# Optimization experiments

Hardware: AMD Instinct MI355X
Metric: run time of the kernel (lower is better)

## Reference

```python
import jax, jax.numpy as jnp
import numpy as np

B, S, H = 1, 2048, 1024
NH, NKV, D = 8, 2, 128           # query heads, kv heads, head_dim
E, TOPK = 64, 6                   # experts per modality, top-k
IT, IV, IS = 512, 256, 1024       # text / vision expert inter, shared inter (=512*2)
THETA = 500000.0
SECTIONS = (22, 22, 20)           # h, w, t rotary freq split; sum = D//2
EPS = 1e-5


def rmsnorm(x, w):
    return x * w * jax.lax.rsqrt(jnp.mean(x * x, axis=-1, keepdims=True) + EPS)


def apply_mrope(x, positions):
    # x: [B,S,h,D]; positions: [3,B,S] (h, w, t position streams)
    inv_freq = 1.0 / (THETA ** (jnp.arange(0, D, 2, dtype=jnp.float32) / D))  # [D//2]
    axis_idx = np.repeat(np.arange(3), SECTIONS)              # which pos stream per freq band
    pos = jnp.transpose(positions[axis_idx], (1, 2, 0)).astype(jnp.float32)  # [B,S,D//2]
    freqs = pos * inv_freq
    cos = jnp.cos(freqs)[:, :, None, :]
    sin = jnp.sin(freqs)[:, :, None, :]
    x1, x2 = x[..., 0::2], x[..., 1::2]                       # interleaved (non-neox)
    o1 = x1 * cos - x2 * sin
    o2 = x1 * sin + x2 * cos
    return jnp.stack([o1, o2], axis=-1).reshape(x.shape)


def attention(x, positions, w_qkv, w_o):
    b, s, _ = x.shape
    qkv = x @ w_qkv
    q, k, v = jnp.split(qkv, [NH * D, NH * D + NKV * D], axis=-1)
    q = q.reshape(b, s, NH, D)
    k = k.reshape(b, s, NKV, D)
    v = v.reshape(b, s, NKV, D)
    q = apply_mrope(q, positions)
    k = apply_mrope(k, positions)
    rep = NH // NKV
    k = jnp.repeat(k, rep, axis=2)
    v = jnp.repeat(v, rep, axis=2)
    scores = jnp.einsum('bqhd,bkhd->bhqk', q, k) * (D ** -0.5)
    causal = jnp.tril(jnp.ones((s, s), bool))
    scores = jnp.where(causal, scores, -jnp.inf)
    attn = jax.nn.softmax(scores, axis=-1)
    out = jnp.einsum('bhqk,bkhd->bqhd', attn, v).reshape(b, s, NH * D)
    return out @ w_o


def mlp(x, wg, wu, wd):
    return (jax.nn.silu(x @ wg) * (x @ wu)) @ wd


def moe_branch(x, gate_w, bias, wg, wu, wd):
    # x: [T,H]; gate_w: [H,E] fp32; bias: [E] fp32 correction bias
    logits = x.astype(jnp.float32) @ gate_w                   # [T,E]
    scores = jax.nn.sigmoid(logits)
    _, topi = jax.lax.top_k(scores + bias[None, :], TOPK)     # bias only picks experts
    w = jnp.take_along_axis(scores, topi, axis=-1)            # weights from raw scores
    w = w / jnp.sum(w, axis=-1, keepdims=True)                # renormalize
    T = x.shape[0]
    gates = jnp.zeros((T, E), jnp.float32).at[jnp.arange(T)[:, None], topi].set(w)
    g = jax.nn.silu(jnp.einsum('th,ehi->eti', x, wg)) * jnp.einsum('th,ehi->eti', x, wu)
    g = g * gates.T[:, :, None].astype(x.dtype)               # fold routing weights pre-down-proj
    return jnp.einsum('eti,eih->th', g, wd)


def _forward(hidden_states, positions, visual_token_mask, w_qkv, w_o, ln1_w, ln2_w,
             text_gate_w, vision_gate_w, corr_bias, tw_gate, tw_up, tw_down,
             vw_gate, vw_up, vw_down, sw_gate, sw_up, sw_down):
    h = hidden_states + attention(rmsnorm(hidden_states, ln1_w), positions, w_qkv, w_o)
    x = rmsnorm(h, ln2_w).reshape(-1, H)                      # [T,H]
    shared = mlp(x, sw_gate, sw_up, sw_down)
    text_out = moe_branch(x, text_gate_w, corr_bias[0], tw_gate, tw_up, tw_down)
    vision_out = moe_branch(x, vision_gate_w, corr_bias[1], vw_gate, vw_up, vw_down)
    mask = visual_token_mask.reshape(-1, 1)
    moe_out = jnp.where(mask, vision_out, text_out) + shared
    return h + moe_out.reshape(h.shape)


def setup_inputs() -> dict:
    key = jax.random.key(0)
    ks = jax.random.split(key, 16)
    rn = lambda i, shape, s: jax.random.normal(ks[i], shape, jnp.float32) * s
    return dict(
        hidden_states=rn(0, (B, S, H), 1.0),
        positions=jnp.broadcast_to(jnp.arange(S, dtype=jnp.int32)[None, None, :], (3, B, S)),
        visual_token_mask=jax.random.bernoulli(ks[1], 0.3, (B, S)),
        w_qkv=rn(2, (H, (NH + 2 * NKV) * D), H ** -0.5),
        w_o=rn(3, (NH * D, H), (NH * D) ** -0.5),
        ln1_w=jnp.ones((H,), jnp.float32),
        ln2_w=jnp.ones((H,), jnp.float32),
        text_gate_w=rn(4, (H, E), H ** -0.5),
        vision_gate_w=rn(5, (H, E), H ** -0.5),
        corr_bias=rn(6, (2, E), 0.02),
        tw_gate=rn(7, (E, H, IT), H ** -0.5),
        tw_up=rn(8, (E, H, IT), H ** -0.5),
        tw_down=rn(9, (E, IT, H), IT ** -0.5),
        vw_gate=rn(10, (E, H, IV), H ** -0.5),
        vw_up=rn(11, (E, H, IV), H ** -0.5),
        vw_down=rn(12, (E, IV, H), IV ** -0.5),
        sw_gate=rn(13, (H, IS), H ** -0.5),
        sw_up=rn(14, (H, IS), H ** -0.5),
        sw_down=rn(15, (IS, H), IS ** -0.5),
    )


def reference(hidden_states, positions, visual_token_mask, w_qkv, w_o, ln1_w, ln2_w,
              text_gate_w, vision_gate_w, corr_bias, tw_gate, tw_up, tw_down,
              vw_gate, vw_up, vw_down, sw_gate, sw_up, sw_down):
    return _forward(hidden_states, positions, visual_token_mask, w_qkv, w_o, ln1_w, ln2_w,
                    text_gate_w, vision_gate_w, corr_bias, tw_gate, tw_up, tw_down,
                    vw_gate, vw_up, vw_down, sw_gate, sw_up, sw_down)
```

## Files before the change

### kernel.cpp

```cpp
#include <hip/hip_runtime.h>
#include <hip/hip_bf16.h>
#include <math.h>

#define TT   2048
#define HID  1024
#define NHEAD 8
#define NKVH  2
#define HD   128
#define QKVN 1536
#define NEXP 64
#define NTOP 6
#define I_T  512
#define I_V  256
#define I_S  1024
#define SBASE ((size_t)12288 * 512)
#define NCHUNK 576

typedef unsigned short u16;
typedef __attribute__((ext_vector_type(8))) short short8v;
typedef __attribute__((ext_vector_type(4))) float f32x4;

__device__ inline u16 f2bf(float f) {
  __hip_bfloat16 h = __float2bfloat16(f);
  return *reinterpret_cast<u16*>(&h);
}
__device__ inline float bfu2f(u16 u) {
  unsigned x = ((unsigned)u) << 16;
  return __uint_as_float(x);
}
__device__ inline void split2(float f, u16& h, u16& l) {
  h = f2bf(f);
  l = f2bf(f - bfu2f(h));
}
__device__ inline void split8(const float* f, u16* h, u16* l) {
#pragma unroll
  for (int i = 0; i < 8; ++i) split2(f[i], h[i], l[i]);
}

__device__ inline f32x4 mfma16(short8v a, short8v b, f32x4 c) {
  return __builtin_amdgcn_mfma_f32_16x16x32_bf16(a, b, c, 0, 0, 0);
}

__device__ inline void wload64(const float* __restrict__ W, int ldw, int c0, int kc,
                               float4* r) {
  const int t = threadIdx.x;
  const int c4 = (t & 15) << 2;
  const int r0 = t >> 4;
#pragma unroll
  for (int j = 0; j < 8; ++j)
    r[j] = *(const float4*)&W[(size_t)(kc + r0 + j * 16) * ldw + c0 + c4];
}
__device__ inline void wwrite64(const float4* r, u16* lds) {
  const int t = threadIdx.x;
  const int c4 = (t & 15) << 2;
  const int r0 = t >> 4;
#pragma unroll
  for (int j = 0; j < 8; ++j) {
    int k = r0 + j * 16;
    u16* dst = lds + ((size_t)(k >> 3) * 64 + c4) * 8 + (k & 7);
    float4 v = r[j];
    dst[0]  = f2bf(v.x);
    dst[8]  = f2bf(v.y);
    dst[16] = f2bf(v.z);
    dst[24] = f2bf(v.w);
  }
}

template<bool F32, bool BF, bool LO>
__global__ __launch_bounds__(256) void rmsnorm_kernel(const float* __restrict__ x,
                                                      const float* __restrict__ w,
                                                      float* __restrict__ o32,
                                                      u16* __restrict__ obfH,
                                                      u16* __restrict__ obfL) {
  const int row = blockIdx.x;
  const int t = threadIdx.x;
  const float4 v = *(const float4*)(x + (size_t)row * HID + t * 4);
  float ss = v.x*v.x + v.y*v.y + v.z*v.z + v.w*v.w;
#pragma unroll
  for (int m = 32; m >= 1; m >>= 1) ss += __shfl_xor(ss, m);
  __shared__ float red[4];
  __shared__ float rrs;
  if ((t & 63) == 0) red[t >> 6] = ss;
  __syncthreads();
  if (t == 0) rrs = rsqrtf((red[0] + red[1] + red[2] + red[3]) * (1.0f / HID) + 1e-5f);
  __syncthreads();
  const float rr = rrs;
  const float4 wv = *(const float4*)(w + t * 4);
  float o[4];
  o[0] = v.x * wv.x * rr; o[1] = v.y * wv.y * rr;
  o[2] = v.z * wv.z * rr; o[3] = v.w * wv.w * rr;
  if (F32) *(float4*)(o32 + (size_t)row * HID + t * 4) = *(float4*)o;
  if (BF) {
    u16 h[4], l[4];
#pragma unroll
    for (int i = 0; i < 4; ++i) split2(o[i], h[i], l[i]);
    *(uint2*)(obfH + (size_t)row * HID + t * 4) = *(uint2*)h;
    if (LO) *(uint2*)(obfL + (size_t)row * HID + t * 4) = *(uint2*)l;
  }
}

__global__ __launch_bounds__(256) void convert_w(const float* __restrict__ W, int N,
                                                 u16* __restrict__ PH,
                                                 u16* __restrict__ PL) {
  const int c = blockIdx.x * 256 + threadIdx.x;
  const int k8 = blockIdx.y;
  float f[8];
#pragma unroll
  for (int e = 0; e < 8; ++e) f[e] = W[(size_t)(k8 * 8 + e) * N + c];
  u16 h8[8], l8[8];
  split8(f, h8, l8);
  size_t gi = ((size_t)(c >> 5) * 128 + k8) * 256 + (size_t)(c & 31) * 8;
  *(uint4*)&PH[gi] = *(uint4*)h8;
  *(uint4*)&PL[gi] = *(uint4*)l8;
}

template<bool RES>
__global__ __launch_bounds__(256) void dense_split(const u16* __restrict__ AH,
                                                   const u16* __restrict__ AL,
                                                   const u16* __restrict__ WPH,
                                                   const u16* __restrict__ WPL,
                                                   const float* __restrict__ resid,
                                                   float* __restrict__ C, int N) {
  __shared__ u16 sWH[32768], sWL[32768];
  __shared__ u16 sAH[4096],  sAL[4096];
  const int t = threadIdx.x;
  const int cs = blockIdx.x;
  const int c0 = cs * 32;
  const int rows = TT / gridDim.y;
  const int mstart = blockIdx.y * rows, mend = mstart + rows;
  {
    const u16* gh = WPH + (size_t)cs * 32768;
    const u16* gl = WPL + (size_t)cs * 32768;
#pragma unroll
    for (int r = 0; r < 16; ++r) {
      int i8 = (t + 256 * r) * 8;
      *(uint4*)&sWH[i8] = *(const uint4*)&gh[i8];
      *(uint4*)&sWL[i8] = *(const uint4*)&gl[i8];
    }
  }
  const int w = t >> 6, lane = t & 63;
  const int rowHalf = (w & 1) << 4, colHalf = (w >> 1) << 4;
  for (int m0 = mstart; m0 < mend; m0 += 32) {
    f32x4 hh = {0.f,0.f,0.f,0.f}, hl = {0.f,0.f,0.f,0.f};
    f32x4 lh = {0.f,0.f,0.f,0.f}, ll = {0.f,0.f,0.f,0.f};
    for (int kc = 0; kc < HID; kc += 128) {
      __syncthreads();
#pragma unroll
      for (int r = 0; r < 2; ++r) {
        int task = t + 256 * r;
        int row = task >> 4, kg = task & 15;
        size_t g = (size_t)(m0 + row) * HID + kc + kg * 8;
        *(uint4*)&sAH[(kg * 32 + row) * 8] = *(const uint4*)&AH[g];
        *(uint4*)&sAL[(kg * 32 + row) * 8] = *(const uint4*)&AL[g];
      }
      __syncthreads();
#pragma unroll
      for (int ks = 0; ks < 4; ++ks) {
        int arow = rowHalf + (lane & 15);
        int akg = ks * 4 + (lane >> 4);
        short8v ah = *(const short8v*)&sAH[(akg * 32 + arow) * 8];
        short8v al = *(const short8v*)&sAL[(akg * 32 + arow) * 8];
        int wcol = colHalf + (lane & 15);
        int wkg = (kc >> 3) + ks * 4 + (lane >> 4);
        short8v bh = *(const short8v*)&sWH[(wkg * 32 + wcol) * 8];
        short8v bl = *(const short8v*)&sWL[(wkg * 32 + wcol) * 8];
        hh = mfma16(ah, bh, hh);
        hl = mfma16(ah, bl, hl);
        lh = mfma16(al, bh, lh);
        ll = mfma16(al, bl, ll);
      }
    }
    f32x4 acc = (hh + hl) + (lh + ll);
#pragma unroll
    for (int i = 0; i < 4; ++i) {
      int r = m0 + rowHalf + ((lane >> 4) << 2) + i;
      int c = c0 + colHalf + (lane & 15);
      float v = acc[i];
      if (RES) v += resid[(size_t)r * N + c];
      C[(size_t)r * N + c] = v;
    }
  }
}

__global__ __launch_bounds__(256) void pack_qkv(const float* __restrict__ qkv,
                                                const int* __restrict__ pos,
                                                u16* __restrict__ Qh, u16* __restrict__ Ql,
                                                u16* __restrict__ Kph, u16* __restrict__ Kpl,
                                                u16* __restrict__ Vph, u16* __restrict__ Vpl) {
  const int tile = blockIdx.x;
  const int t = threadIdx.x;
  __shared__ float cs[2048], sn[2048];
  for (int i = t; i < 2048; i += 256) {
    int tok32 = i >> 6, fi = i & 63;
    int tok = tile * 32 + tok32;
    int axis = (fi < 22) ? 0 : (fi < 44 ? 1 : 2);
    float posv = (float)pos[axis * TT + tok];
    float invf = powf(500000.0f, -((float)(2 * fi)) / 128.0f);
    float ang = posv * invf;
    sincosf(ang, &sn[i], &cs[i]);
  }
  __syncthreads();
  for (int task = t; task < 4096; task += 256) {
    int h = task >> 9;
    int rem = task & 511;
    int tok32 = rem >> 4, fi4 = rem & 15;
    int tok = tile * 32 + tok32;
    const float* src = qkv + (size_t)tok * QKVN + h * HD + fi4 * 8;
    float4 v0 = *(const float4*)src, v1 = *(const float4*)(src + 4);
    float f[8] = {v0.x, v0.y, v0.z, v0.w, v1.x, v1.y, v1.z, v1.w};
    float o[8];
#pragma unroll
    for (int j = 0; j < 4; ++j) {
      int fi = fi4 * 4 + j;
      float c = cs[tok32 * 64 + fi], s = sn[tok32 * 64 + fi];
      o[2*j]   = f[2*j] * c - f[2*j+1] * s;
      o[2*j+1] = f[2*j] * s + f[2*j+1] * c;
    }
    u16 h8[8], l8[8];
    split8(o, h8, l8);
    size_t d = (size_t)tok * HID + h * HD + fi4 * 8;
    *(uint4*)&Qh[d] = *(uint4*)h8;
    *(uint4*)&Ql[d] = *(uint4*)l8;
  }
  for (int task = t; task < 1024; task += 256) {
    int kvh = task >> 9;
    int rem = task & 511;
    int kk = rem >> 4, fi4 = rem & 15;
    int tok = tile * 32 + kk;
    const float* src = qkv + (size_t)tok * QKVN + NHEAD * HD + kvh * HD + fi4 * 8;
    float4 v0 = *(const float4*)src, v1 = *(const float4*)(src + 4);
    float f[8] = {v0.x, v0.y, v0.z, v0.w, v1.x, v1.y, v1.z, v1.w};
    float o[8];
#pragma unroll
    for (int j = 0; j < 4; ++j) {
      int fi = fi4 * 4 + j;
      float c = cs[kk * 64 + fi], s = sn[kk * 64 + fi];
      o[2*j]   = f[2*j] * c - f[2*j+1] * s;
      o[2*j+1] = f[2*j] * s + f[2*j+1] * c;
    }
    u16 h8[8], l8[8];
    split8(o, h8, l8);
    size_t d = ((size_t)(kvh * 64 + tile) << 12) + (size_t)(fi4 * 32 + kk) * 8;
    *(uint4*)&Kph[d] = *(uint4*)h8;
    *(uint4*)&Kpl[d] = *(uint4*)l8;
  }
  for (int task = t; task < 1024; task += 256) {
    int kvh = task >> 9;
    int rem = task & 511;
    int g = rem >> 7, dcol = rem & 127;
    float f[8];
#pragma unroll
    for (int e = 0; e < 8; ++e) {
      int key = ((e >> 2) * 16) + g * 4 + (e & 3);
      f[e] = qkv[(size_t)(tile * 32 + key) * QKVN + (NHEAD + NKVH) * HD + kvh * HD + dcol];
    }
    u16 h8[8], l8[8];
    split8(f, h8, l8);
    size_t d = ((size_t)(kvh * 64 + tile) << 12) + (size_t)(g * 128 + dcol) * 8;
    *(uint4*)&Vph[d] = *(uint4*)h8;
    *(uint4*)&Vpl[d] = *(uint4*)l8;
  }
}

__global__ void chunk_setup(int* __restrict__ tab, int* __restrict__ startOff) {
  if (threadIdx.x == 0 && blockIdx.x == 0) {
    int idx = 0;
    for (int qb = 0; qb < TT / 16; ++qb) {
      startOff[qb] = idx;
      int nkt = (qb >> 1) + 1;
      int nch = (nkt + 7) >> 3;
      for (int c = 0; c < nch; ++c) { tab[idx] = qb * 16 + c; ++idx; }
    }
  }
}

__global__ __launch_bounds__(256) void attn_part(const u16* __restrict__ Qh,
                                                 const u16* __restrict__ Ql,
                                                 const u16* __restrict__ Kph,
                                                 const u16* __restrict__ Kpl,
                                                 const u16* __restrict__ Vph,
                                                 const u16* __restrict__ Vpl,
                                                 const int* __restrict__ tab,
                                                 float* __restrict__ Opart,
                                                 float* __restrict__ Mpart,
                                                 float* __restrict__ Lpart) {
  const int ci = blockIdx.x;
  const int kvh = blockIdx.y;
  const int w = threadIdx.x >> 6, lane = threadIdx.x & 63;
  const int head = kvh * 4 + w;
  const int ent = tab[ci];
  const int qb = ent >> 4, cc = ent & 15;
  const int qw0 = qb * 16;
  const int lrow = lane & 15, loct = lane >> 4;
  const int nkt = (qb >> 1) + 1;
  const int kt0 = cc * 8, kt1 = min(kt0 + 8, nkt);

  short8v qh[4], ql[4];
  {
    const size_t qoff = (size_t)(qw0 + lrow) * HID + head * HD + loct * 8;
#pragma unroll
    for (int dc = 0; dc < 4; ++dc) {
      qh[dc] = *(const short8v*)&Qh[qoff + dc * 32];
      ql[dc] = *(const short8v*)&Ql[qoff + dc * 32];
    }
  }

  f32x4 o[8];
#pragma unroll
  for (int dt = 0; dt < 8; ++dt) o[dt] = (f32x4){0.f,0.f,0.f,0.f};
  float mr = -INFINITY, lr = 0.f;
  const float scale = 0.08838834764831845f;

  for (int kt = kt0; kt < kt1; ++kt) {
    const int kv0 = kt * 32;
    const size_t tb = ((size_t)(kvh * 64 + kt) << 12);
    const u16* kbh = Kph + tb;
    const u16* kbl = Kpl + tb;
    f32x4 s[2];
    __builtin_amdgcn_s_setprio(1);
#pragma unroll
    for (int nt = 0; nt < 2; ++nt) {
      f32x4 shh = {0.f,0.f,0.f,0.f}, shl = {0.f,0.f,0.f,0.f};
      f32x4 slh = {0.f,0.f,0.f,0.f};
#pragma unroll
      for (int dc = 0; dc < 4; ++dc) {
        int off = ((dc * 4 + loct) * 32 + nt * 16 + lrow) * 8;
        short8v kh = *(const short8v*)&kbh[off];
        short8v kl = *(const short8v*)&kbl[off];
        shh = mfma16(kh, qh[dc], shh);
        shl = mfma16(kh, ql[dc], shl);
        slh = mfma16(kl, qh[dc], slh);
      }
      s[nt] = shh + (shl + slh);
    }
    __builtin_amdgcn_s_setprio(0);
    const int qrow = qw0 + lrow;
    float rmax = -INFINITY;
#pragma unroll
    for (int nt = 0; nt < 2; ++nt)
#pragma unroll
      for (int i = 0; i < 4; ++i) {
        int key = kv0 + nt * 16 + loct * 4 + i;
        float v = s[nt][i] * scale;
        s[nt][i] = (key <= qrow) ? v : -INFINITY;
        rmax = fmaxf(rmax, s[nt][i]);
      }
    rmax = fmaxf(rmax, __shfl_xor(rmax, 16));
    rmax = fmaxf(rmax, __shfl_xor(rmax, 32));
    const float mn = fmaxf(mr, rmax);
    const float corr = expf(mr - mn);
    mr = mn;
    float p[2][4];
    float ps = 0.f;
#pragma unroll
    for (int nt = 0; nt < 2; ++nt)
#pragma unroll
      for (int i = 0; i < 4; ++i) { p[nt][i] = expf(s[nt][i] - mr); ps += p[nt][i]; }
    ps += __shfl_xor(ps, 16);
    ps += __shfl_xor(ps, 32);
    lr = lr * corr + ps;
#pragma unroll
    for (int dt = 0; dt < 8; ++dt)
#pragma unroll
      for (int i = 0; i < 4; ++i) o[dt][i] *= corr;
    u16 ph8[8], pl8[8];
#pragma unroll
    for (int j = 0; j < 8; ++j) split2(p[j >> 2][j & 3], ph8[j], pl8[j]);
    short8v pfh = *(short8v*)ph8;
    short8v pfl = *(short8v*)pl8;
    const u16* vbh = Vph + tb;
    const u16* vbl = Vpl + tb;
    __builtin_amdgcn_s_setprio(1);
#pragma unroll
    for (int dt = 0; dt < 8; ++dt) {
      int off = (loct * 128 + dt * 16 + lrow) * 8;
      short8v vh = *(const short8v*)&vbh[off];
      short8v vl = *(const short8v*)&vbl[off];
      o[dt] = mfma16(vh, pfh, o[dt]);
      o[dt] = mfma16(vh, pfl, o[dt]);
      o[dt] = mfma16(vl, pfh, o[dt]);
    }
    __builtin_amdgcn_s_setprio(0);
  }
  const size_t ob = (size_t)head * NCHUNK + ci;
  float* op = Opart + ob * 2048;
#pragma unroll
  for (int dt = 0; dt < 8; ++dt)
#pragma unroll
    for (int i = 0; i < 4; ++i) {
      int d = dt * 16 + loct * 4 + i;
      op[d * 16 + lrow] = o[dt][i];
    }
  if (loct == 0) {
    Mpart[ob * 16 + lrow] = mr;
    Lpart[ob * 16 + lrow] = lr;
  }
}

__global__ __launch_bounds__(256) void attn_combine(const float* __restrict__ Opart,
                                                    const float* __restrict__ Mpart,
                                                    const float* __restrict__ Lpart,
                                                    const int* __restrict__ startOff,
                                                    u16* __restrict__ aoH,
                                                    u16* __restrict__ aoL) {
  const int qb = blockIdx.x, head = blockIdx.y;
  const int t = threadIdx.x;
  const int row = t >> 4, c8 = (t & 15) * 8;
  const int nkt = (qb >> 1) + 1;
  const int nch = (nkt + 7) >> 3;
  const int s0 = startOff[qb];
  const size_t hb = (size_t)head * NCHUNK;
  float M = -INFINITY;
  for (int ch = 0; ch < nch; ++ch)
    M = fmaxf(M, Mpart[(hb + s0 + ch) * 16 + row]);
  float L = 0.f;
  float acc[8];
#pragma unroll
  for (int j = 0; j < 8; ++j) acc[j] = 0.f;
  for (int ch = 0; ch < nch; ++ch) {
    const size_t cb = hb + s0 + ch;
    float sc = expf(Mpart[cb * 16 + row] - M);
    L += sc * Lpart[cb * 16 + row];
    const float* op = Opart + cb * 2048;
#pragma unroll
    for (int j = 0; j < 8; ++j)
      acc[j] += sc * op[(c8 + j) * 16 + row];
  }
  const float inv = 1.f / L;
  u16 h8[8], l8[8];
  float f[8];
#pragma unroll
  for (int j = 0; j < 8; ++j) f[j] = acc[j] * inv;
  split8(f, h8, l8);
  const size_t d = (size_t)(qb * 16 + row) * HID + head * HD + c8;
  *(uint4*)&aoH[d] = *(uint4*)h8;
  *(uint4*)&aoL[d] = *(uint4*)l8;
}

__global__ __launch_bounds__(256) void gate_kernel(const float* __restrict__ x2,
                                                   const int* __restrict__ vmask,
                                                   const float* __restrict__ tg,
                                                   const float* __restrict__ vg,
                                                   const float* __restrict__ cbias,
                                                   int* __restrict__ counts,
                                                   int* __restrict__ ptok,
                                                   float* __restrict__ pw) {
  const int tok = blockIdx.x;
  const int t = threadIdx.x;
  __shared__ float xs[HID];
  __shared__ float part[4][NEXP];
  __shared__ float sc[NEXP];
  __shared__ float sb[NEXP];
  *(float4*)&xs[t * 4] = *(const float4*)(x2 + (size_t)tok * HID + t * 4);
  __syncthreads();
  const int vis = (vmask[tok] != 0) ? 1 : 0;
  const float* gw = vis ? vg : tg;
  {
    const int e = t & 63, pr = t >> 6;
    float acc = 0.f;
    for (int h = pr * 256; h < (pr + 1) * 256; ++h) acc += xs[h] * gw[h * NEXP + e];
    part[pr][e] = acc;
  }
  __syncthreads();
  if (t < NEXP) {
    float a = part[0][t] + part[1][t] + part[2][t] + part[3][t];
    float s = 1.f / (1.f + expf(-a));
    sc[t] = s;
    sb[t] = s + cbias[vis * NEXP + t];
  }
  __syncthreads();
  if (t == 0) {
    int chosen[NTOP];
    unsigned long long usedm = 0ULL;
    float wsum = 0.f;
    for (int k = 0; k < NTOP; ++k) {
      float best = -1e30f; int bi = 0;
      for (int e = 0; e < NEXP; ++e) {
        if ((usedm >> e) & 1ULL) continue;
        if (sb[e] > best) { best = sb[e]; bi = e; }
      }
      usedm |= (1ULL << bi);
      chosen[k] = bi;
      wsum += sc[bi];
    }
    const float inv = 1.f / wsum;
    for (int k = 0; k < NTOP; ++k) {
      int e = chosen[k];
      int slot = vis * NEXP + e;
      int pos = atomicAdd(&counts[slot], 1);
      ptok[slot * TT + pos] = tok;
      pw[slot * TT + pos] = sc[e] * inv;
    }
  }
}

__global__ void scan_kernel(const int* __restrict__ counts, int* __restrict__ rowoff) {
  if (threadIdx.x == 0 && blockIdx.x == 0) {
    int s = 0;
    for (int i = 0; i < 128; ++i) { rowoff[i] = s; s += counts[i]; }
    rowoff[128] = s;
  }
}

template<int MODE>
__device__ inline void act_base(const int* rowoff, int slot, size_t& eb, int& stride) {
  if (MODE == 0) { eb = (size_t)rowoff[slot] * 512; stride = 512; }
  else if (MODE == 1) {
    int Rt = rowoff[64];
    eb = (size_t)Rt * 512 + (size_t)(rowoff[slot] - Rt) * 256; stride = 256;
  } else { eb = SBASE; stride = 1024; }
}

template<int IDIM, int MODE>
__global__ __launch_bounds__(256) void gateup_stream(const u16* __restrict__ X,
                                                     const float* __restrict__ WG,
                                                     const float* __restrict__ WU,
                                                     const int* __restrict__ counts,
                                                     const int* __restrict__ ptok,
                                                     const float* __restrict__ pw,
                                                     const int* __restrict__ rowoff,
                                                     u16* __restrict__ ACT) {
  __shared__ u16 sG[2][8192], sU[2][8192];
  __shared__ int toksL[256];
  __shared__ float twsL[256];
  const int c0 = blockIdx.x * 64;
  int cnt, mstart, mend, slot = 0;
  size_t eb; int stride;
  const float *wgp, *wup;
  if (MODE == 2) {
    cnt = TT; mstart = blockIdx.y * 256; mend = mstart + 256;
    eb = SBASE; stride = 1024;
    wgp = WG; wup = WU;
  } else {
    const int e = blockIdx.y;
    slot = (MODE == 1 ? NEXP : 0) + e;
    cnt = counts[slot];
    mstart = 0; mend = cnt;
    act_base<MODE>(rowoff, slot, eb, stride);
    wgp = WG + (size_t)e * HID * IDIM;
    wup = WU + (size_t)e * HID * IDIM;
  }
  if (mstart >= mend) return;
  const int w = threadIdx.x >> 6, lane = threadIdx.x & 63;
  const int lrow = lane & 15, loct = lane >> 4;

  for (int m0 = mstart; m0 < mend; m0 += 256) {
    {
      int gi = m0 + threadIdx.x;
      int tok = 0; float tw = 0.f;
      if (gi < cnt) {
        tok = (MODE == 2) ? gi : ptok[slot * TT + gi];
        tw  = (MODE == 2) ? 1.f : pw[slot * TT + gi];
      }
      toksL[threadIdx.x] = tok; twsL[threadIdx.x] = tw;
    }
    float4 rg[8], ru[8];
    wload64(wgp, IDIM, c0, 0, rg);
    wload64(wup, IDIM, c0, 0, ru);
    __syncthreads();
    wwrite64(rg, sG[0]);
    wwrite64(ru, sU[0]);
    const u16* xr[4];
#pragma unroll
    for (int tt = 0; tt < 4; ++tt)
      xr[tt] = X + (size_t)toksL[(w + tt * 4) * 16 + lrow] * HID;
    f32x4 aG[4][4], aU[4][4];
#pragma unroll
    for (int tt = 0; tt < 4; ++tt)
#pragma unroll
      for (int cf = 0; cf < 4; ++cf) {
        aG[tt][cf] = (f32x4){0.f,0.f,0.f,0.f};
        aU[tt][cf] = (f32x4){0.f,0.f,0.f,0.f};
      }
    __syncthreads();
    for (int c = 0; c < HID / 128; ++c) {
      const int cur = c & 1;
      if (c + 1 < HID / 128) {
        wload64(wgp, IDIM, c0, (c + 1) * 128, rg);
        wload64(wup, IDIM, c0, (c + 1) * 128, ru);
      }
#pragma unroll
      for (int ks = 0; ks < 4; ++ks) {
        short8v a[4];
#pragma unroll
        for (int tt = 0; tt < 4; ++tt)
          a[tt] = *(const short8v*)&xr[tt][c * 128 + ks * 32 + loct * 8];
        const int gbase = ((ks * 4 + loct) * 64 + lrow) * 8;
#pragma unroll
        for (int cf = 0; cf < 4; ++cf) {
          short8v bg = *(const short8v*)&sG[cur][gbase + cf * 128];
          short8v bu = *(const short8v*)&sU[cur][gbase + cf * 128];
#pragma unroll
          for (int tt = 0; tt < 4; ++tt) {
            aG[tt][cf] = mfma16(a[tt], bg, aG[tt][cf]);
            aU[tt][cf] = mfma16(a[tt], bu, aU[tt][cf]);
          }
        }
      }
      if (c + 1 < HID / 128) {
        wwrite64(rg, sG[cur ^ 1]);
        wwrite64(ru, sU[cur ^ 1]);
      }
      __syncthreads();
    }
#pragma unroll
    for (int tt = 0; tt < 4; ++tt) {
      const int ti = w + tt * 4;
#pragma unroll
      for (int i = 0; i < 4; ++i) {
        const int r = loct * 4 + i;
        const int gi = m0 + ti * 16 + r;
        if (gi < cnt) {
          const float twv = twsL[ti * 16 + r];
#pragma unroll
          for (int cf = 0; cf < 4; ++cf) {
            float g = aG[tt][cf][i], u = aU[tt][cf][i];
            float a = g / (1.f + expf(-g)) * u * twv;
            ACT[eb + (size_t)gi * stride + c0 + cf * 16 + lrow] = f2bf(a);
          }
        }
      }
    }
    __syncthreads();
  }
}

template<int KDIM, int MODE>
__global__ __launch_bounds__(256) void down_stream(const u16* __restrict__ ACT,
                                                   const float* __restrict__ WD,
                                                   const int* __restrict__ counts,
                                                   const int* __restrict__ ptok,
                                                   const int* __restrict__ rowoff,
                                                   float* __restrict__ OUT) {
  __shared__ u16 sW[2][8192];
  __shared__ int toksL[256];
  const int c0 = blockIdx.x * 64;
  int cnt, mstart, mend, slot = 0;
  size_t eb; int stride;
  const float* wdp;
  if (MODE == 2) {
    cnt = TT; mstart = blockIdx.y * 256; mend = mstart + 256;
    eb = SBASE; stride = 1024;
    wdp = WD;
  } else {
    const int e = blockIdx.y;
    slot = (MODE == 1 ? NEXP : 0) + e;
    cnt = counts[slot];
    mstart = 0; mend = cnt;
    act_base<MODE>(rowoff, slot, eb, stride);
    wdp = WD + (size_t)e * KDIM * HID;
  }
  if (mstart >= mend) return;
  const int w = threadIdx.x >> 6, lane = threadIdx.x & 63;
  const int lrow = lane & 15, loct = lane >> 4;
  constexpr int NC = KDIM / 128;

  for (int m0 = mstart; m0 < mend; m0 += 256) {
    {
      int gi = m0 + threadIdx.x;
      int tok = 0;
      if (gi < cnt) tok = (MODE == 2) ? gi : ptok[slot * TT + gi];
      toksL[threadIdx.x] = tok;
    }
    float4 rw[8];
    wload64(wdp, HID, c0, 0, rw);
    __syncthreads();
    wwrite64(rw, sW[0]);
    const u16* ar[4];
#pragma unroll
    for (int tt = 0; tt < 4; ++tt) {
      int gi = m0 + (w + tt * 4) * 16 + lrow;
      int gc = (gi < cnt) ? gi : (cnt - 1);
      ar[tt] = ACT + eb + (size_t)gc * stride;
    }
    f32x4 acc[4][4];
#pragma unroll
    for (int tt = 0; tt < 4; ++tt)
#pragma unroll
      for (int cf = 0; cf < 4; ++cf) acc[tt][cf] = (f32x4){0.f,0.f,0.f,0.f};
    __syncthreads();
    for (int c = 0; c < NC; ++c) {
      const int cur = c & 1;
      if (c + 1 < NC) wload64(wdp, HID, c0, (c + 1) * 128, rw);
#pragma unroll
      for (int ks = 0; ks < 4; ++ks) {
        short8v a[4];
#pragma unroll
        for (int tt = 0; tt < 4; ++tt)
          a[tt] = *(const short8v*)&ar[tt][c * 128 + ks * 32 + loct * 8];
        const int gbase = ((ks * 4 + loct) * 64 + lrow) * 8;
#pragma unroll
        for (int cf = 0; cf < 4; ++cf) {
          short8v b = *(const short8v*)&sW[cur][gbase + cf * 128];
#pragma unroll
          for (int tt = 0; tt < 4; ++tt)
            acc[tt][cf] = mfma16(a[tt], b, acc[tt][cf]);
        }
      }
      if (c + 1 < NC) wwrite64(rw, sW[cur ^ 1]);
      __syncthreads();
    }
#pragma unroll
    for (int tt = 0; tt < 4; ++tt) {
      const int ti = w + tt * 4;
#pragma unroll
      for (int i = 0; i < 4; ++i) {
        const int r = loct * 4 + i;
        const int gi = m0 + ti * 16 + r;
        if (gi < cnt) {
          const int tok = toksL[ti * 16 + r];
#pragma unroll
          for (int cf = 0; cf < 4; ++cf)
            atomicAdd(&OUT[(size_t)tok * HID + c0 + cf * 16 + lrow], acc[tt][cf][i]);
        }
      }
    }
    __syncthreads();
  }
}

__global__ __launch_bounds__(256) void add2_kernel(const float* __restrict__ a,
                                                   const float* __restrict__ b,
                                                   float* __restrict__ out) {
  const size_t i = ((size_t)blockIdx.x * 256 + threadIdx.x) * 4;
  const float4 va = *(const float4*)(a + i);
  const float4 vb = *(const float4*)(b + i);
  float4 o;
  o.x = va.x + vb.x; o.y = va.y + vb.y; o.z = va.z + vb.z; o.w = va.w + vb.w;
  *(float4*)(out + i) = o;
}

extern "C" void kernel_launch(void* const* d_in, const int* in_sizes, int n_in,
                              void* d_out, int out_size, void* d_ws, size_t ws_size,
                              hipStream_t stream) {
  const float* hidden   = (const float*)d_in[0];
  const int*   positions= (const int*)d_in[1];
  const int*   vmask    = (const int*)d_in[2];
  const float* w_qkv    = (const float*)d_in[3];
  const float* w_o      = (const float*)d_in[4];
  const float* ln1      = (const float*)d_in[5];
  const float* ln2      = (const float*)d_in[6];
  const float* tgw      = (const float*)d_in[7];
  const float* vgw      = (const float*)d_in[8];
  const float* cbias    = (const float*)d_in[9];
  const float* twg      = (const float*)d_in[10];
  const float* twu      = (const float*)d_in[11];
  const float* twd      = (const float*)d_in[12];
  const float* vwg      = (const float*)d_in[13];
  const float* vwu      = (const float*)d_in[14];
  const float* vwd      = (const float*)d_in[15];
  const float* swg      = (const float*)d_in[16];
  const float* swu      = (const float*)d_in[17];
  const float* swd      = (const float*)d_in[18];
  float* out = (float*)d_out;

  char* ws = (char*)d_ws;
  size_t off = 0;
  auto alloc = [&](size_t bytes) -> void* {
    void* p = ws + off;
    off += (bytes + 255) & ~(size_t)255;
    return p;
  };
  u16*   xbh   = (u16*)alloc((size_t)TT * HID * 2);
  u16*   xbl   = (u16*)alloc((size_t)TT * HID * 2);
  float* qkv   = (float*)alloc((size_t)TT * QKVN * 4);
  u16*   aoH   = (u16*)alloc((size_t)TT * HID * 2);
  u16*   aoL   = (u16*)alloc((size_t)TT * HID * 2);
  float* hbuf  = (float*)alloc((size_t)TT * HID * 4);
  float* x2    = (float*)alloc((size_t)TT * HID * 4);
  u16*   xb2   = (u16*)alloc((size_t)TT * HID * 2);
  float* moe   = (float*)alloc((size_t)TT * HID * 4);
  u16*   ACT   = (u16*)alloc((SBASE + (size_t)TT * 1024) * 2);
  u16*   wqkvPH= (u16*)alloc((size_t)HID * QKVN * 2);
  u16*   wqkvPL= (u16*)alloc((size_t)HID * QKVN * 2);
  u16*   woPH  = (u16*)alloc((size_t)HID * HID * 2);
  u16*   woPL  = (u16*)alloc((size_t)HID * HID * 2);
  u16*   Qph   = (u16*)alloc((size_t)TT * HID * 2);
  u16*   Qpl   = (u16*)alloc((size_t)TT * HID * 2);
  u16*   Kph   = (u16*)alloc((size_t)NKVH * TT * HD * 2);
  u16*   Kpl   = (u16*)alloc((size_t)NKVH * TT * HD * 2);
  u16*   Vph   = (u16*)alloc((size_t)NKVH * TT * HD * 2);
  u16*   Vpl   = (u16*)alloc((size_t)NKVH * TT * HD * 2);
  float* Opart = (float*)alloc((size_t)NHEAD * NCHUNK * 16 * 128 * 4);
  float* Mpart = (float*)alloc((size_t)NHEAD * NCHUNK * 16 * 4);
  float* Lpart = (float*)alloc((size_t)NHEAD * NCHUNK * 16 * 4);
  int*   ctab  = (int*)alloc(NCHUNK * 4);
  int*   cstart= (int*)alloc((TT / 16) * 4);
  int*   counts= (int*)alloc(128 * 4);
  int*   rowoff= (int*)alloc(129 * 4);
  int*   ptok  = (int*)alloc((size_t)128 * TT * 4);
  float* pwgt  = (float*)alloc((size_t)128 * TT * 4);

  hipMemsetAsync(counts, 0, 128 * 4, stream);
  hipMemsetAsync(moe, 0, (size_t)TT * HID * 4, stream);

  chunk_setup<<<1, 64, 0, stream>>>(ctab, cstart);
  convert_w<<<dim3(QKVN / 256, 128), 256, 0, stream>>>(w_qkv, QKVN, wqkvPH, wqkvPL);
  convert_w<<<dim3(HID / 256, 128), 256, 0, stream>>>(w_o, HID, woPH, woPL);

  rmsnorm_kernel<false, true, true><<<TT, 256, 0, stream>>>(hidden, ln1, nullptr, xbh, xbl);
  dense_split<false><<<dim3(QKVN / 32, 8), 256, 0, stream>>>(xbh, xbl, wqkvPH, wqkvPL, nullptr, qkv, QKVN);
  pack_qkv<<<TT / 32, 256, 0, stream>>>(qkv, positions, Qph, Qpl, Kph, Kpl, Vph, Vpl);
  attn_part<<<dim3(NCHUNK, NKVH), 256, 0, stream>>>(Qph, Qpl, Kph, Kpl, Vph, Vpl, ctab, Opart, Mpart, Lpart);
  attn_combine<<<dim3(TT / 16, NHEAD), 256, 0, stream>>>(Opart, Mpart, Lpart, cstart, aoH, aoL);
  dense_split<true><<<dim3(HID / 32, 8), 256, 0, stream>>>(aoH, aoL, woPH, woPL, hidden, hbuf, HID);
  rmsnorm_kernel<true, true, false><<<TT, 256, 0, stream>>>(hbuf, ln2, x2, xb2, nullptr);
  gate_kernel<<<TT, 256, 0, stream>>>(x2, vmask, tgw, vgw, cbias, counts, ptok, pwgt);
  scan_kernel<<<1, 64, 0, stream>>>(counts, rowoff);

  gateup_stream<I_S, 2><<<dim3(I_S / 64, 8), 256, 0, stream>>>(xb2, swg, swu, nullptr, nullptr, nullptr, rowoff, ACT);
  gateup_stream<I_T, 0><<<dim3(I_T / 64, NEXP), 256, 0, stream>>>(xb2, twg, twu, counts, ptok, pwgt, rowoff, ACT);
  gateup_stream<I_V, 1><<<dim3(I_V / 64, NEXP), 256, 0, stream>>>(xb2, vwg, vwu, counts, ptok, pwgt, rowoff, ACT);

  down_stream<I_S, 2><<<dim3(HID / 64, 8), 256, 0, stream>>>(ACT, swd, nullptr, nullptr, rowoff, moe);
  down_stream<I_T, 0><<<dim3(HID / 64, NEXP), 256, 0, stream>>>(ACT, twd, counts, ptok, rowoff, moe);
  down_stream<I_V, 1><<<dim3(HID / 64, NEXP), 256, 0, stream>>>(ACT, vwd, counts, ptok, rowoff, moe);

  add2_kernel<<<(TT * HID) / 1024, 256, 0, stream>>>(hbuf, moe, out);
}
```

Before: 796.9 us.

## Fuse weight bf16 split into streaming dense GEMM with larger register tiles

Removes the separate convert_w passes that pre-split the QKV and output projection weights into hi/lo bf16 packed buffers. The dense GEMM now streams fp32 weights directly, converting them to hi/lo bf16 in LDS one 128-deep K chunk at a time, with the next chunk's global load issued before the current chunk's MFMAs. Each block now computes a 128x64 output tile, with each wave holding a 2x4 grid of 16x16 MFMA accumulators. A operands are read straight from global memory instead of being staged in LDS. This cuts two kernel launches and their extra weight traffic, and the grid becomes 2D over rows and columns instead of keeping a whole column slice of weights resident. The trade-off is that every block redoes the weight conversion, and the A reads from global are uncoalesced per lane.

```diff
diff --git a/kernel.cpp b/kernel.cpp
--- a/kernel.cpp
+++ b/kernel.cpp
@@ -63,6 +63,22 @@
     dst[8]  = f2bf(v.y);
     dst[16] = f2bf(v.z);
     dst[24] = f2bf(v.w);
+  }
+}
+__device__ inline void wwrite64hl(const float4* r, u16* ldsH, u16* ldsL) {
+  const int t = threadIdx.x;
+  const int c4 = (t & 15) << 2;
+  const int r0 = t >> 4;
+#pragma unroll
+  for (int j = 0; j < 8; ++j) {
+    int k = r0 + j * 16;
+    size_t base = ((size_t)(k >> 3) * 64 + c4) * 8 + (k & 7);
+    float4 v = r[j];
+    u16 h, l;
+    split2(v.x, h, l); ldsH[base]      = h; ldsL[base]      = l;
+    split2(v.y, h, l); ldsH[base + 8]  = h; ldsL[base + 8]  = l;
+    split2(v.z, h, l); ldsH[base + 16] = h; ldsL[base + 16] = l;
+    split2(v.w, h, l); ldsH[base + 24] = h; ldsL[base + 24] = l;
   }
 }
 
@@ -99,87 +115,72 @@
   }
 }
 
-__global__ __launch_bounds__(256) void convert_w(const float* __restrict__ W, int N,
-                                                 u16* __restrict__ PH,
-                                                 u16* __restrict__ PL) {
-  const int c = blockIdx.x * 256 + threadIdx.x;
-  const int k8 = blockIdx.y;
-  float f[8];
-#pragma unroll
-  for (int e = 0; e < 8; ++e) f[e] = W[(size_t)(k8 * 8 + e) * N + c];
-  u16 h8[8], l8[8];
-  split8(f, h8, l8);
-  size_t gi = ((size_t)(c >> 5) * 128 + k8) * 256 + (size_t)(c & 31) * 8;
-  *(uint4*)&PH[gi] = *(uint4*)h8;
-  *(uint4*)&PL[gi] = *(uint4*)l8;
-}
-
 template<bool RES>
-__global__ __launch_bounds__(256) void dense_split(const u16* __restrict__ AH,
-                                                   const u16* __restrict__ AL,
-                                                   const u16* __restrict__ WPH,
-                                                   const u16* __restrict__ WPL,
-                                                   const float* __restrict__ resid,
-                                                   float* __restrict__ C, int N) {
-  __shared__ u16 sWH[32768], sWL[32768];
-  __shared__ u16 sAH[4096],  sAL[4096];
-  const int t = threadIdx.x;
-  const int cs = blockIdx.x;
-  const int c0 = cs * 32;
-  const int rows = TT / gridDim.y;
-  const int mstart = blockIdx.y * rows, mend = mstart + rows;
-  {
-    const u16* gh = WPH + (size_t)cs * 32768;
-    const u16* gl = WPL + (size_t)cs * 32768;
-#pragma unroll
-    for (int r = 0; r < 16; ++r) {
-      int i8 = (t + 256 * r) * 8;
-      *(uint4*)&sWH[i8] = *(const uint4*)&gh[i8];
-      *(uint4*)&sWL[i8] = *(const uint4*)&gl[i8];
-    }
-  }
-  const int w = t >> 6, lane = t & 63;
-  const int rowHalf = (w & 1) << 4, colHalf = (w >> 1) << 4;
-  for (int m0 = mstart; m0 < mend; m0 += 32) {
-    f32x4 hh = {0.f,0.f,0.f,0.f}, hl = {0.f,0.f,0.f,0.f};
-    f32x4 lh = {0.f,0.f,0.f,0.f}, ll = {0.f,0.f,0.f,0.f};
-    for (int kc = 0; kc < HID; kc += 128) {
+__global__ __launch_bounds__(256) void dense_stream(const u16* __restrict__ AH,
+                                                    const u16* __restrict__ AL,
+                                                    const float* __restrict__ W,
+                                                    const float* __restrict__ resid,
+                                                    float* __restrict__ C, int N) {
+  __shared__ u16 sWH[8192], sWL[8192];
+  const int c0 = blockIdx.x * 64;
+  const int m0 = blockIdx.y * 128;
+  const int w = threadIdx.x >> 6, lane = threadIdx.x & 63;
+  const int lrow = lane & 15, loct = lane >> 4;
+  const int rbase = m0 + w * 32;
+
+  f32x4 acc[2][4];
+#pragma unroll
+  for (int rt = 0; rt < 2; ++rt)
+#pragma unroll
+    for (int cf = 0; cf < 4; ++cf) acc[rt][cf] = (f32x4){0.f,0.f,0.f,0.f};
+
+  float4 rw[8];
+  wload64(W, N, c0, 0, rw);
+  wwrite64hl(rw, sWH, sWL);
+  __syncthreads();
+  for (int c = 0; c < 8; ++c) {
+    if (c + 1 < 8) wload64(W, N, c0, (c + 1) * 128, rw);
+#pragma unroll
+    for (int ks = 0; ks < 4; ++ks) {
+      short8v ah[2], al[2];
+#pragma unroll
+      for (int rt = 0; rt < 2; ++rt) {
+        size_t g = (size_t)(rbase + rt * 16 + lrow) * HID + c * 128 + ks * 32 + loct * 8;
+        ah[rt] = *(const short8v*)&AH[g];
+        al[rt] = *(const short8v*)&AL[g];
+      }
+      const int gbase = ((ks * 4 + loct) * 64 + lrow) * 8;
+#pragma unroll
+      for (int cf = 0; cf < 4; ++cf) {
+        short8v bh = *(const short8v*)&sWH[gbase + cf * 128];
+        short8v bl = *(const short8v*)&sWL[gbase + cf * 128];
+#pragma unroll
+        for (int rt = 0; rt < 2; ++rt) {
+          acc[rt][cf] = mfma16(ah[rt], bh, acc[rt][cf]);
+          acc[rt][cf] = mfma16(ah[rt], bl, acc[rt][cf]);
+          acc[rt][cf] = mfma16(al[rt], bh, acc[rt][cf]);
+          acc[rt][cf] = mfma16(al[rt], bl, acc[rt][cf]);
+        }
+      }
+    }
+    __syncthreads();
+    if (c + 1 < 8) {
+      wwrite64hl(rw, sWH, sWL);
       __syncthreads();
-#pragma unroll
-      for (int r = 0; r < 2; ++r) {
-        int task = t + 256 * r;
-        int row = task >> 4, kg = task & 15;
-        size_t g = (size_t)(m0 + row) * HID + kc + kg * 8;
-        *(uint4*)&sAH[(kg * 32 + row) * 8] = *(const uint4*)&AH[g];
-        *(uint4*)&sAL[(kg * 32 + row) * 8] = *(const uint4*)&AL[g];
-      }
-      __syncthreads();
-#pragma unroll
-      for (int ks = 0; ks < 4; ++ks) {
-        int arow = rowHalf + (lane & 15);
-        int akg = ks * 4 + (lane >> 4);
-        short8v ah = *(const short8v*)&sAH[(akg * 32 + arow) * 8];
-        short8v al = *(const short8v*)&sAL[(akg * 32 + arow) * 8];
-        int wcol = colHalf + (lane & 15);
-        int wkg = (kc >> 3) + ks * 4 + (lane >> 4);
-        short8v bh = *(const short8v*)&sWH[(wkg * 32 + wcol) * 8];
-        short8v bl = *(const short8v*)&sWL[(wkg * 32 + wcol) * 8];
-        hh = mfma16(ah, bh, hh);
-        hl = mfma16(ah, bl, hl);
-        lh = mfma16(al, bh, lh);
-        ll = mfma16(al, bl, ll);
-      }
-    }
-    f32x4 acc = (hh + hl) + (lh + ll);
-#pragma unroll
-    for (int i = 0; i < 4; ++i) {
-      int r = m0 + rowHalf + ((lane >> 4) << 2) + i;
-      int c = c0 + colHalf + (lane & 15);
-      float v = acc[i];
-      if (RES) v += resid[(size_t)r * N + c];
-      C[(size_t)r * N + c] = v;
-    }
-  }
+    }
+  }
+#pragma unroll
+  for (int rt = 0; rt < 2; ++rt)
+#pragma unroll
+    for (int cf = 0; cf < 4; ++cf)
+#pragma unroll
+      for (int i = 0; i < 4; ++i) {
+        int row = rbase + rt * 16 + loct * 4 + i;
+        int col = c0 + cf * 16 + lrow;
+        float v = acc[rt][cf][i];
+        if (RES) v += resid[(size_t)row * N + col];
+        C[(size_t)row * N + col] = v;
+      }
 }
 
 __global__ __launch_bounds__(256) void pack_qkv(const float* __restrict__ qkv,
@@ -771,10 +772,6 @@
   u16*   xb2   = (u16*)alloc((size_t)TT * HID * 2);
   float* moe   = (float*)alloc((size_t)TT * HID * 4);
   u16*   ACT   = (u16*)alloc((SBASE + (size_t)TT * 1024) * 2);
-  u16*   wqkvPH= (u16*)alloc((size_t)HID * QKVN * 2);
-  u16*   wqkvPL= (u16*)alloc((size_t)HID * QKVN * 2);
-  u16*   woPH  = (u16*)alloc((size_t)HID * HID * 2);
-  u16*   woPL  = (u16*)alloc((size_t)HID * HID * 2);
   u16*   Qph   = (u16*)alloc((size_t)TT * HID * 2);
   u16*   Qpl   = (u16*)alloc((size_t)TT * HID * 2);
   u16*   Kph   = (u16*)alloc((size_t)NKVH * TT * HD * 2);
@@ -795,15 +792,13 @@
   hipMemsetAsync(moe, 0, (size_t)TT * HID * 4, stream);
 
   chunk_setup<<<1, 64, 0, stream>>>(ctab, cstart);
-  convert_w<<<dim3(QKVN / 256, 128), 256, 0, stream>>>(w_qkv, QKVN, wqkvPH, wqkvPL);
-  convert_w<<<dim3(HID / 256, 128), 256, 0, stream>>>(w_o, HID, woPH, woPL);
 
   rmsnorm_kernel<false, true, true><<<TT, 256, 0, stream>>>(hidden, ln1, nullptr, xbh, xbl);
-  dense_split<false><<<dim3(QKVN / 32, 8), 256, 0, stream>>>(xbh, xbl, wqkvPH, wqkvPL, nullptr, qkv, QKVN);
+  dense_stream<false><<<dim3(QKVN / 64, TT / 128), 256, 0, stream>>>(xbh, xbl, w_qkv, nullptr, qkv, QKVN);
   pack_qkv<<<TT / 32, 256, 0, stream>>>(qkv, positions, Qph, Qpl, Kph, Kpl, Vph, Vpl);
   attn_part<<<dim3(NCHUNK, NKVH), 256, 0, stream>>>(Qph, Qpl, Kph, Kpl, Vph, Vpl, ctab, Opart, Mpart, Lpart);
   attn_combine<<<dim3(TT / 16, NHEAD), 256, 0, stream>>>(Opart, Mpart, Lpart, cstart, aoH, aoL);
-  dense_split<true><<<dim3(HID / 32, 8), 256, 0, stream>>>(aoH, aoL, woPH, woPL, hidden, hbuf, HID);
+  dense_stream<true><<<dim3(HID / 64, TT / 128), 256, 0, stream>>>(aoH, aoL, w_o, hidden, hbuf, HID);
   rmsnorm_kernel<true, true, false><<<TT, 256, 0, stream>>>(hbuf, ln2, x2, xb2, nullptr);
   gate_kernel<<<TT, 256, 0, stream>>>(x2, vmask, tgw, vgw, cbias, counts, ptok, pwgt);
   scan_kernel<<<1, 64, 0, stream>>>(counts, rowoff);
```

After: 706.0 us. -11.4%, faster.
